# Kernel optimization log

Measured on AMD Instinct MI355X. Metric: run time of the kernel, lower is better.

## Reference

```python
import jax, jax.numpy as jnp
import numpy as np

N_NODES = 50000
N_EDGES = 600000
IN_FEATS, HID_FEATS, OUT_FEATS = 128, 128, 64


def setup_inputs() -> dict:
    key = jax.random.key(0)
    ks = jax.random.split(key, 6)
    x = jax.random.normal(ks[0], (N_NODES, IN_FEATS), dtype=jnp.float32)
    src = jax.random.randint(ks[1], (N_EDGES,), 0, N_NODES, dtype=jnp.int32)
    dst = jax.random.randint(ks[2], (N_EDGES,), 0, N_NODES, dtype=jnp.int32)
    # Xavier-ish init for the two fc_neigh linear layers
    W1 = jax.random.normal(ks[3], (IN_FEATS, HID_FEATS), dtype=jnp.float32) * (1.0 / np.sqrt(IN_FEATS))
    b1 = jnp.zeros((HID_FEATS,), dtype=jnp.float32)
    W2 = jax.random.normal(ks[4], (HID_FEATS, OUT_FEATS), dtype=jnp.float32) * (1.0 / np.sqrt(HID_FEATS))
    b2 = jnp.zeros((OUT_FEATS,), dtype=jnp.float32)
    return {"x": x, "src": src, "dst": dst, "W1": W1, "b1": b1, "W2": W2, "b2": b2}


def _sage_gcn_layer(h, src, dst, W, b, deg):
    # DGL SAGEConv(aggregator_type='gcn'):
    #   h_neigh[i] = (sum_{j in in-nbrs(i)} h[j] + h[i]) / (in_deg[i] + 1)
    #   out = h_neigh @ W + b   (no separate fc_self for 'gcn')
    msg_sum = jax.ops.segment_sum(h[src], dst, num_segments=N_NODES)  # [N, d]
    h_neigh = (msg_sum + h) / (deg + 1.0)[:, None]
    return h_neigh @ W + b


def reference(x, src, dst, W1, b1, W2, b2):
    # in-degree per destination node (shared by both layers)
    deg = jax.ops.segment_sum(jnp.ones_like(dst, dtype=x.dtype), dst, num_segments=N_NODES)  # [N]
    h = _sage_gcn_layer(x, src, dst, W1, b1, deg)
    h = jax.nn.relu(h)
    h = _sage_gcn_layer(h, src, dst, W2, b2, deg)
    return h
```

## Files before the change

### kernel.cpp

```cpp
#include <hip/hip_runtime.h>

#define NF 128

typedef __attribute__((ext_vector_type(8))) short short8;
typedef __attribute__((ext_vector_type(4))) float f32x4;

__device__ inline ushort f2bf(float f) {
    uint u = __float_as_uint(f);
    return (ushort)((u + 0x7FFFu + ((u >> 16) & 1u)) >> 16);
}
__device__ inline float bf2f(ushort u) {
    return __uint_as_float(((uint)u) << 16);
}

__global__ __launch_bounds__(256) void zero_kernel(int4* __restrict__ p, int n4) {
    int i = blockIdx.x * 256 + threadIdx.x;
    int stride = gridDim.x * 256;
    int4 z = make_int4(0, 0, 0, 0);
    for (; i < n4; i += stride) p[i] = z;
}

__global__ void hist_kernel(const int* __restrict__ dst, int* __restrict__ cnt,
                            int n_edges) {
    int i = blockIdx.x * blockDim.x + threadIdx.x;
    if (i < n_edges) atomicAdd(&cnt[dst[i]], 1);
}

__global__ __launch_bounds__(256) void reduce_kernel(const int* __restrict__ cnt,
                                                     int* __restrict__ partials,
                                                     int n) {
    __shared__ int s[256];
    int t = threadIdx.x;
    int i = blockIdx.x * 256 + t;
    s[t] = (i < n) ? cnt[i] : 0;
    __syncthreads();
    for (int off = 128; off > 0; off >>= 1) {
        if (t < off) s[t] += s[t + off];
        __syncthreads();
    }
    if (t == 0) partials[blockIdx.x] = s[0];
}

__global__ __launch_bounds__(256) void scan_partials_kernel(int* __restrict__ partials,
                                                            int nb) {
    __shared__ int s[256];
    int t = threadIdx.x;
    int carry = 0;
    for (int base = 0; base < nb; base += 256) {
        int v = (base + t < nb) ? partials[base + t] : 0;
        s[t] = v;
        __syncthreads();
        for (int off = 1; off < 256; off <<= 1) {
            int a = (t >= off) ? s[t - off] : 0;
            __syncthreads();
            s[t] += a;
            __syncthreads();
        }
        if (base + t < nb) partials[base + t] = carry + s[t] - v;
        int total = s[255];
        __syncthreads();
        carry += total;
    }
}

__global__ __launch_bounds__(256) void scan_apply_kernel(int* __restrict__ cnt,
                                                         int* __restrict__ rowptr,
                                                         const int* __restrict__ partials,
                                                         int n) {
    __shared__ int s[256];
    int t = threadIdx.x;
    int i = blockIdx.x * 256 + t;
    int v = (i < n) ? cnt[i] : 0;
    s[t] = v;
    __syncthreads();
    for (int off = 1; off < 256; off <<= 1) {
        int a = (t >= off) ? s[t - off] : 0;
        __syncthreads();
        s[t] += a;
        __syncthreads();
    }
    int off0 = partials[blockIdx.x];
    if (i < n) {
        rowptr[i + 1] = off0 + s[t];
        cnt[i] = off0 + s[t] - v;
    }
    if (blockIdx.x == 0 && t == 0) rowptr[0] = 0;
}

__global__ void fill_kernel(const int* __restrict__ src,
                            const int* __restrict__ dst,
                            int* __restrict__ cursor,
                            int* __restrict__ edge_src, int n_edges) {
    int i = blockIdx.x * blockDim.x + threadIdx.x;
    if (i < n_edges) {
        int slot = atomicAdd(&cursor[dst[i]], 1);
        edge_src[slot] = src[i];
    }
}

__global__ __launch_bounds__(256) void prep_w_kernel(const float* __restrict__ W1,
                                                     const float* __restrict__ W2,
                                                     ushort* __restrict__ W1t,
                                                     ushort* __restrict__ W2t) {
    int t = blockIdx.x * 256 + threadIdx.x;
    if (t < 128 * 128) {
        int k = t >> 7, n = t & 127;
        W1t[n * NF + k] = f2bf(W1[t]);
    }
    if (t < 64 * 128) {
        int k = t >> 6, n = t & 63;
        W2t[n * NF + k] = f2bf(W2[k * 64 + n]);
    }
}

__global__ __launch_bounds__(256) void f2bf_kernel(const float* __restrict__ in,
                                                   ushort* __restrict__ out, int n8) {
    int i = blockIdx.x * 256 + threadIdx.x;
    if (i >= n8) return;
    const float4* in4 = reinterpret_cast<const float4*>(in);
    float4 v0 = in4[i * 2], v1 = in4[i * 2 + 1];
    short8 o;
    o[0] = (short)f2bf(v0.x); o[1] = (short)f2bf(v0.y);
    o[2] = (short)f2bf(v0.z); o[3] = (short)f2bf(v0.w);
    o[4] = (short)f2bf(v1.x); o[5] = (short)f2bf(v1.y);
    o[6] = (short)f2bf(v1.z); o[7] = (short)f2bf(v1.w);
    *reinterpret_cast<short8*>(&out[i * 8]) = o;
}

__global__ __launch_bounds__(256) void aggregate_kernel(
    const ushort* __restrict__ hb, const int* __restrict__ rowptr,
    const int* __restrict__ edge_src, ushort* __restrict__ hn, int n_nodes) {
    int t = threadIdx.x;
    int g = t & 31;
    int node = blockIdx.x * 8 + (t >> 5);
    if (node >= n_nodes) return;
    const ushort4* h4 = reinterpret_cast<const ushort4*>(hb);
    int e0 = rowptr[node], e1 = rowptr[node + 1];
    ushort4 sv = h4[(size_t)node * 32 + g];
    float a0x = bf2f(sv.x), a0y = bf2f(sv.y), a0z = bf2f(sv.z), a0w = bf2f(sv.w);
    float a1x = 0.f, a1y = 0.f, a1z = 0.f, a1w = 0.f;
    float a2x = 0.f, a2y = 0.f, a2z = 0.f, a2w = 0.f;
    float a3x = 0.f, a3y = 0.f, a3z = 0.f, a3w = 0.f;
    for (int base = e0; base < e1; base += 32) {
        int m = min(32, e1 - base);
        int sg = (base + g < e1) ? edge_src[base + g] : 0;
        int j = 0;
        for (; j + 4 <= m; j += 4) {
            int s0 = __shfl(sg, j, 32);
            int s1 = __shfl(sg, j + 1, 32);
            int s2 = __shfl(sg, j + 2, 32);
            int s3 = __shfl(sg, j + 3, 32);
            ushort4 v0 = h4[(size_t)s0 * 32 + g];
            ushort4 v1 = h4[(size_t)s1 * 32 + g];
            ushort4 v2 = h4[(size_t)s2 * 32 + g];
            ushort4 v3 = h4[(size_t)s3 * 32 + g];
            a0x += bf2f(v0.x); a0y += bf2f(v0.y); a0z += bf2f(v0.z); a0w += bf2f(v0.w);
            a1x += bf2f(v1.x); a1y += bf2f(v1.y); a1z += bf2f(v1.z); a1w += bf2f(v1.w);
            a2x += bf2f(v2.x); a2y += bf2f(v2.y); a2z += bf2f(v2.z); a2w += bf2f(v2.w);
            a3x += bf2f(v3.x); a3y += bf2f(v3.y); a3z += bf2f(v3.z); a3w += bf2f(v3.w);
        }
        for (; j < m; ++j) {
            int s = __shfl(sg, j, 32);
            ushort4 v = h4[(size_t)s * 32 + g];
            a0x += bf2f(v.x); a0y += bf2f(v.y); a0z += bf2f(v.z); a0w += bf2f(v.w);
        }
    }
    float inv = 1.0f / (float)(e1 - e0 + 1);
    ushort4 o;
    o.x = f2bf((a0x + a1x + a2x + a3x) * inv);
    o.y = f2bf((a0y + a1y + a2y + a3y) * inv);
    o.z = f2bf((a0z + a1z + a2z + a3z) * inv);
    o.w = f2bf((a0w + a1w + a2w + a3w) * inv);
    reinterpret_cast<ushort4*>(hn)[(size_t)node * 32 + g] = o;
}

template <int OUTW, bool RELU, bool BF16OUT>
__global__ __launch_bounds__(256) void gemm_mfma_kernel(
    const ushort* __restrict__ A, const ushort* __restrict__ Wt,
    const float* __restrict__ bias, void* __restrict__ out_v, int n_nodes) {
    constexpr int NT = OUTW / 16;
    __shared__ ushort As[64][136];
    __shared__ ushort Ws[OUTW][136];

    int t = threadIdx.x;
    int row0 = blockIdx.x * 64;
    for (int i = t; i < 64 * 16; i += 256) {
        int r = i >> 4, c = i & 15;
        int gr = row0 + r;
        short8 v = {};
        if (gr < n_nodes)
            v = *reinterpret_cast<const short8*>(&A[(size_t)gr * NF + c * 8]);
        *reinterpret_cast<short8*>(&As[r][c * 8]) = v;
    }
    for (int i = t; i < OUTW * 16; i += 256) {
        int r = i >> 4, c = i & 15;
        *reinterpret_cast<short8*>(&Ws[r][c * 8]) =
            *reinterpret_cast<const short8*>(&Wt[r * NF + c * 8]);
    }
    __syncthreads();

    int w = t >> 6;
    int l = t & 63;
    int m16 = l & 15;
    int g = l >> 4;
    int m0 = w * 16;

    f32x4 acc[NT];
#pragma unroll
    for (int nt = 0; nt < NT; nt++) acc[nt] = {0.f, 0.f, 0.f, 0.f};

#pragma unroll
    for (int kk = 0; kk < 4; kk++) {
        int k0 = kk * 32 + g * 8;
        short8 a = *reinterpret_cast<const short8*>(&As[m0 + m16][k0]);
#pragma unroll
        for (int nt = 0; nt < NT; nt++) {
            short8 b = *reinterpret_cast<const short8*>(&Ws[nt * 16 + m16][k0]);
            acc[nt] = __builtin_amdgcn_mfma_f32_16x16x32_bf16(a, b, acc[nt], 0, 0, 0);
        }
    }

#pragma unroll
    for (int nt = 0; nt < NT; nt++) {
        int col = nt * 16 + m16;
        float bv = bias[col];
#pragma unroll
        for (int i = 0; i < 4; i++) {
            int gr = row0 + m0 + g * 4 + i;
            if (gr < n_nodes) {
                float v = acc[nt][i] + bv;
                if (RELU) v = fmaxf(v, 0.f);
                if (BF16OUT)
                    ((ushort*)out_v)[(size_t)gr * OUTW + col] = f2bf(v);
                else
                    ((float*)out_v)[(size_t)gr * OUTW + col] = v;
            }
        }
    }
}

extern "C" void kernel_launch(void* const* d_in, const int* in_sizes, int n_in,
                              void* d_out, int out_size, void* d_ws, size_t ws_size,
                              hipStream_t stream) {
    const float* x   = (const float*)d_in[0];
    const int*   src = (const int*)d_in[1];
    const int*   dst = (const int*)d_in[2];
    const float* W1  = (const float*)d_in[3];
    const float* b1  = (const float*)d_in[4];
    const float* W2  = (const float*)d_in[5];
    const float* b2  = (const float*)d_in[6];
    float* out = (float*)d_out;

    const int n_nodes = in_sizes[0] / NF;
    const int n_edges = in_sizes[1];
    const int nb = (n_nodes + 255) / 256;

    int* rowptr   = (int*)d_ws;
    int* cnt      = rowptr + (n_nodes + 4);
    int* edge_src = cnt + n_nodes;
    int* partials = edge_src + n_edges;
    size_t iw = (size_t)(n_nodes + 4) + n_nodes + n_edges + nb;
    iw = (iw + 63) & ~(size_t)63;
    ushort* W1t = (ushort*)((int*)d_ws + iw);
    ushort* W2t = W1t + 128 * NF;
    ushort* xb  = W2t + 64 * NF;
    ushort* hn  = xb + (size_t)n_nodes * NF;
    ushort* hbuf = hn + (size_t)n_nodes * NF;

    zero_kernel<<<50, 256, 0, stream>>>((int4*)cnt, n_nodes / 4);

    int eb = (n_edges + 255) / 256;
    hist_kernel<<<eb, 256, 0, stream>>>(dst, cnt, n_edges);
    reduce_kernel<<<nb, 256, 0, stream>>>(cnt, partials, n_nodes);
    scan_partials_kernel<<<1, 256, 0, stream>>>(partials, nb);
    scan_apply_kernel<<<nb, 256, 0, stream>>>(cnt, rowptr, partials, n_nodes);
    fill_kernel<<<eb, 256, 0, stream>>>(src, dst, cnt, edge_src, n_edges);
    prep_w_kernel<<<64, 256, 0, stream>>>(W1, W2, W1t, W2t);

    int n8 = n_nodes * NF / 8;
    f2bf_kernel<<<(n8 + 255) / 256, 256, 0, stream>>>(x, xb, n8);

    int ab = (n_nodes + 7) / 8;
    int gb = (n_nodes + 63) / 64;

    aggregate_kernel<<<ab, 256, 0, stream>>>(xb, rowptr, edge_src, hn, n_nodes);
    gemm_mfma_kernel<128, true, true><<<gb, 256, 0, stream>>>(hn, W1t, b1, hbuf, n_nodes);
    aggregate_kernel<<<ab, 256, 0, stream>>>(hbuf, rowptr, edge_src, hn, n_nodes);
    gemm_mfma_kernel<64, false, false><<<gb, 256, 0, stream>>>(hn, W2t, b2, out, n_nodes);
}
```

Baseline: 158.0 us.

## Reorder second layer to transform before aggregating and merge prep kernels

Uses linearity to apply the second layer's weight matrix before neighbor aggregation, so the gather for layer two reads 64-wide bf16 rows instead of 128-wide. A new 64-feature aggregation kernel adds the bias and writes the fp32 output. It also merges the weight-transpose kernel and the x-to-bf16 conversion into one launch. The output is now rounded to bf16 before aggregation, which adds another rounding step, and a new intermediate buffer is needed in the workspace.

After: 151.9 us. 1.04x faster.

```diff
diff --git a/kernel.cpp b/kernel.cpp
--- a/kernel.cpp
+++ b/kernel.cpp
@@ -98,33 +98,33 @@
     }
 }
 
-__global__ __launch_bounds__(256) void prep_w_kernel(const float* __restrict__ W1,
-                                                     const float* __restrict__ W2,
-                                                     ushort* __restrict__ W1t,
-                                                     ushort* __restrict__ W2t) {
-    int t = blockIdx.x * 256 + threadIdx.x;
-    if (t < 128 * 128) {
-        int k = t >> 7, n = t & 127;
-        W1t[n * NF + k] = f2bf(W1[t]);
-    }
-    if (t < 64 * 128) {
-        int k = t >> 6, n = t & 63;
-        W2t[n * NF + k] = f2bf(W2[k * 64 + n]);
-    }
-}
-
-__global__ __launch_bounds__(256) void f2bf_kernel(const float* __restrict__ in,
-                                                   ushort* __restrict__ out, int n8) {
-    int i = blockIdx.x * 256 + threadIdx.x;
-    if (i >= n8) return;
-    const float4* in4 = reinterpret_cast<const float4*>(in);
-    float4 v0 = in4[i * 2], v1 = in4[i * 2 + 1];
-    short8 o;
-    o[0] = (short)f2bf(v0.x); o[1] = (short)f2bf(v0.y);
-    o[2] = (short)f2bf(v0.z); o[3] = (short)f2bf(v0.w);
-    o[4] = (short)f2bf(v1.x); o[5] = (short)f2bf(v1.y);
-    o[6] = (short)f2bf(v1.z); o[7] = (short)f2bf(v1.w);
-    *reinterpret_cast<short8*>(&out[i * 8]) = o;
+__global__ __launch_bounds__(256) void prep_kernel(
+    const float* __restrict__ x, const float* __restrict__ W1,
+    const float* __restrict__ W2, ushort* __restrict__ xb,
+    ushort* __restrict__ W1t, ushort* __restrict__ W2t, int n8) {
+    int b = blockIdx.x;
+    if (b < 64) {
+        int t = b * 256 + threadIdx.x;
+        if (t < 128 * 128) {
+            int k = t >> 7, n = t & 127;
+            W1t[n * NF + k] = f2bf(W1[t]);
+        }
+        if (t < 64 * 128) {
+            int k = t >> 6, n = t & 63;
+            W2t[n * NF + k] = f2bf(W2[k * 64 + n]);
+        }
+    } else {
+        int i = (b - 64) * 256 + threadIdx.x;
+        if (i >= n8) return;
+        const float4* in4 = reinterpret_cast<const float4*>(x);
+        float4 v0 = in4[i * 2], v1 = in4[i * 2 + 1];
+        short8 o;
+        o[0] = (short)f2bf(v0.x); o[1] = (short)f2bf(v0.y);
+        o[2] = (short)f2bf(v0.z); o[3] = (short)f2bf(v0.w);
+        o[4] = (short)f2bf(v1.x); o[5] = (short)f2bf(v1.y);
+        o[6] = (short)f2bf(v1.z); o[7] = (short)f2bf(v1.w);
+        *reinterpret_cast<short8*>(&xb[i * 8]) = o;
+    }
 }
 
 __global__ __launch_bounds__(256) void aggregate_kernel(
@@ -174,7 +174,56 @@
     reinterpret_cast<ushort4*>(hn)[(size_t)node * 32 + g] = o;
 }
 
-template <int OUTW, bool RELU, bool BF16OUT>
+__global__ __launch_bounds__(256) void aggregate64_kernel(
+    const ushort* __restrict__ y, const int* __restrict__ rowptr,
+    const int* __restrict__ edge_src, const float* __restrict__ b,
+    float* __restrict__ out, int n_nodes) {
+    int t = threadIdx.x;
+    int g = t & 15;
+    int node = blockIdx.x * 16 + (t >> 4);
+    if (node >= n_nodes) return;
+    const ushort4* y4 = reinterpret_cast<const ushort4*>(y);
+    int e0 = rowptr[node], e1 = rowptr[node + 1];
+    ushort4 sv = y4[(size_t)node * 16 + g];
+    float a0x = bf2f(sv.x), a0y = bf2f(sv.y), a0z = bf2f(sv.z), a0w = bf2f(sv.w);
+    float a1x = 0.f, a1y = 0.f, a1z = 0.f, a1w = 0.f;
+    float a2x = 0.f, a2y = 0.f, a2z = 0.f, a2w = 0.f;
+    float a3x = 0.f, a3y = 0.f, a3z = 0.f, a3w = 0.f;
+    for (int base = e0; base < e1; base += 16) {
+        int m = min(16, e1 - base);
+        int sg = (base + g < e1) ? edge_src[base + g] : 0;
+        int j = 0;
+        for (; j + 4 <= m; j += 4) {
+            int s0 = __shfl(sg, j, 16);
+            int s1 = __shfl(sg, j + 1, 16);
+            int s2 = __shfl(sg, j + 2, 16);
+            int s3 = __shfl(sg, j + 3, 16);
+            ushort4 v0 = y4[(size_t)s0 * 16 + g];
+            ushort4 v1 = y4[(size_t)s1 * 16 + g];
+            ushort4 v2 = y4[(size_t)s2 * 16 + g];
+            ushort4 v3 = y4[(size_t)s3 * 16 + g];
+            a0x += bf2f(v0.x); a0y += bf2f(v0.y); a0z += bf2f(v0.z); a0w += bf2f(v0.w);
+            a1x += bf2f(v1.x); a1y += bf2f(v1.y); a1z += bf2f(v1.z); a1w += bf2f(v1.w);
+            a2x += bf2f(v2.x); a2y += bf2f(v2.y); a2z += bf2f(v2.z); a2w += bf2f(v2.w);
+            a3x += bf2f(v3.x); a3y += bf2f(v3.y); a3z += bf2f(v3.z); a3w += bf2f(v3.w);
+        }
+        for (; j < m; ++j) {
+            int s = __shfl(sg, j, 16);
+            ushort4 v = y4[(size_t)s * 16 + g];
+            a0x += bf2f(v.x); a0y += bf2f(v.y); a0z += bf2f(v.z); a0w += bf2f(v.w);
+        }
+    }
+    float inv = 1.0f / (float)(e1 - e0 + 1);
+    float4 bv = reinterpret_cast<const float4*>(b)[g];
+    float4 o;
+    o.x = (a0x + a1x + a2x + a3x) * inv + bv.x;
+    o.y = (a0y + a1y + a2y + a3y) * inv + bv.y;
+    o.z = (a0z + a1z + a2z + a3z) * inv + bv.z;
+    o.w = (a0w + a1w + a2w + a3w) * inv + bv.w;
+    reinterpret_cast<float4*>(out)[(size_t)node * 16 + g] = o;
+}
+
+template <int OUTW, bool RELU, bool BF16OUT, bool BIAS>
 __global__ __launch_bounds__(256) void gemm_mfma_kernel(
     const ushort* __restrict__ A, const ushort* __restrict__ Wt,
     const float* __restrict__ bias, void* __restrict__ out_v, int n_nodes) {
@@ -223,7 +272,7 @@
 #pragma unroll
     for (int nt = 0; nt < NT; nt++) {
         int col = nt * 16 + m16;
-        float bv = bias[col];
+        float bv = BIAS ? bias[col] : 0.f;
 #pragma unroll
         for (int i = 0; i < 4; i++) {
             int gr = row0 + m0 + g * 4 + i;
@@ -261,11 +310,12 @@
     int* partials = edge_src + n_edges;
     size_t iw = (size_t)(n_nodes + 4) + n_nodes + n_edges + nb;
     iw = (iw + 63) & ~(size_t)63;
-    ushort* W1t = (ushort*)((int*)d_ws + iw);
-    ushort* W2t = W1t + 128 * NF;
-    ushort* xb  = W2t + 64 * NF;
-    ushort* hn  = xb + (size_t)n_nodes * NF;
+    ushort* W1t  = (ushort*)((int*)d_ws + iw);
+    ushort* W2t  = W1t + 128 * NF;
+    ushort* xb   = W2t + 64 * NF;
+    ushort* hn   = xb + (size_t)n_nodes * NF;
     ushort* hbuf = hn + (size_t)n_nodes * NF;
+    ushort* y    = hbuf + (size_t)n_nodes * NF;
 
     zero_kernel<<<50, 256, 0, stream>>>((int4*)cnt, n_nodes / 4);
 
@@ -275,16 +325,15 @@
     scan_partials_kernel<<<1, 256, 0, stream>>>(partials, nb);
     scan_apply_kernel<<<nb, 256, 0, stream>>>(cnt, rowptr, partials, n_nodes);
     fill_kernel<<<eb, 256, 0, stream>>>(src, dst, cnt, edge_src, n_edges);
-    prep_w_kernel<<<64, 256, 0, stream>>>(W1, W2, W1t, W2t);
 
     int n8 = n_nodes * NF / 8;
-    f2bf_kernel<<<(n8 + 255) / 256, 256, 0, stream>>>(x, xb, n8);
+    prep_kernel<<<64 + (n8 + 255) / 256, 256, 0, stream>>>(x, W1, W2, xb, W1t, W2t, n8);
 
     int ab = (n_nodes + 7) / 8;
     int gb = (n_nodes + 63) / 64;
 
     aggregate_kernel<<<ab, 256, 0, stream>>>(xb, rowptr, edge_src, hn, n_nodes);
-    gemm_mfma_kernel<128, true, true><<<gb, 256, 0, stream>>>(hn, W1t, b1, hbuf, n_nodes);
-    aggregate_kernel<<<ab, 256, 0, stream>>>(hbuf, rowptr, edge_src, hn, n_nodes);
-    gemm_mfma_kernel<64, false, false><<<gb, 256, 0, stream>>>(hn, W2t, b2, out, n_nodes);
-}
+    gemm_mfma_kernel<128, true, true, true><<<gb, 256, 0, stream>>>(hn, W1t, b1, hbuf, n_nodes);
+    gemm_mfma_kernel<64, false, true, false><<<gb, 256, 0, stream>>>(hbuf, W2t, nullptr, y, n_nodes);
+    aggregate64_kernel<<<(n_nodes + 15) / 16, 256, 0, stream>>>(y, rowptr, edge_src, b2, out, n_nodes);
+}
```
